# Kernel optimization log

Measured on AMD Instinct MI355X. Metric: run time of the kernel, lower is better.

Reference implementation:

```python
import jax, jax.numpy as jnp
import numpy as np

# Production GravNet config: 8 events x 4096 hits, K=40 neighbours, 4 spatial dims
B, V, K, S, P, F_IN, F_OUT = 8, 4096, 40, 4, 64, 64, 128
N = B * V
MAX_RADIUS_SQ = 1.0  # SelectKnn(max_radius=1.0)


def setup_inputs() -> dict:
    key = jax.random.key(0)
    ks = jax.random.split(key, 7)
    x = jax.random.normal(ks[0], (N, F_IN), jnp.float32)
    # Dense layer params (glorot-ish scaling)
    W_prop = jax.random.normal(ks[1], (F_IN, P), jnp.float32) / np.sqrt(F_IN)
    b_prop = jnp.zeros((P,), jnp.float32)
    W_sp = jax.random.normal(ks[2], (F_IN, S), jnp.float32) / np.sqrt(F_IN)
    b_sp = jnp.zeros((S,), jnp.float32)
    # output transform input dim = n_prop_total (2*P) + F_IN
    W_out = jax.random.normal(ks[3], (2 * P + F_IN, F_OUT), jnp.float32) / np.sqrt(2 * P + F_IN)
    b_out = jnp.zeros((F_OUT,), jnp.float32)
    row_splits = jnp.arange(B + 1, dtype=jnp.int32) * V  # equal-size ragged segments
    return dict(x=x, W_prop=W_prop, b_prop=b_prop, W_sp=W_sp, b_sp=b_sp,
                W_out=W_out, b_out=b_out, row_splits=row_splits)


def _knn_indices(coords):
    """Per-event brute-force KNN. coords: [N,S] -> global neighbour idx [N,K]."""
    c = coords.reshape(B, V, S)
    # pairwise squared distances within each event: [B,V,V]
    d = jnp.sum((c[:, :, None, :] - c[:, None, :, :]) ** 2, axis=-1)
    neg_d, idx = jax.lax.top_k(-d, K + 1)  # nearest first; col 0 is self (d=0)
    idx, dsq = idx[:, :, 1:], -neg_d[:, :, 1:]
    # tf_compatible max_radius: out-of-radius neighbours -> self index
    self_idx = jnp.arange(V, dtype=idx.dtype)[None, :, None]
    idx = jnp.where(dsq > MAX_RADIUS_SQ, self_idx, idx)
    gidx = idx + (jnp.arange(B, dtype=idx.dtype) * V)[:, None, None]
    return gidx.reshape(N, K)


def reference(x, W_prop, b_prop, W_sp, b_sp, W_out, b_out, row_splits):
    coords = x @ W_sp + b_sp                      # [N,S] learned coordinates
    nidx = _knn_indices(coords)                   # [N,K] (int, non-diff)
    nb_coords = coords[nidx]                      # [N,K,S] gather
    dsq = jnp.sum((coords[:, None, :] - nb_coords) ** 2, axis=-1)  # [N,K]
    feat = x @ W_prop + b_prop                    # [N,P]
    w = jnp.exp(-10.0 * dsq)[:, :, None]          # gauss_of_lin(10*d^2)
    nf = feat[nidx] * w                           # [N,K,P]
    agg = jnp.concatenate([nf.max(axis=1), nf.mean(axis=1)], axis=-1)  # [N,2P]
    out = jnp.tanh(jnp.concatenate([agg, x], axis=-1) @ W_out + b_out)  # [N,F_OUT]
    return out
```

## Files before the change

### kernel.cpp

```cpp
#include <hip/hip_runtime.h>
#include <cstdint>
#include <cstddef>

#define NB   8
#define VV   4096
#define KNN  40
#define NTOT 32768
#define CAP  224
#define INFB 0x7F800000u
#define ONEB 0x3F800000u

__device__ __forceinline__ int xbucket(float x) {
  int b = (int)floorf((x + 4.f) * 32.f);
  return b < 0 ? 0 : (b > 255 ? 255 : b);
}

__global__ __launch_bounds__(256) void k_prep(
    const float* __restrict__ x, const float* __restrict__ W_prop,
    const float* __restrict__ b_prop, const float* __restrict__ W_sp,
    const float* __restrict__ b_sp, const float* __restrict__ W_out,
    float* __restrict__ coords, float* __restrict__ feat,
    float* __restrict__ xW, int* __restrict__ hist)
{
  __shared__ float xt[64][64];
  const int t = threadIdx.x;
  const int row0 = blockIdx.x * 64;

  #pragma unroll
  for (int i = 0; i < 16; ++i) {
    int idx = t + i * 256;
    xt[idx >> 6][idx & 63] = x[(size_t)row0 * 64 + idx];
  }
  __syncthreads();

  {
    const int col = t & 63, rb = (t >> 6) * 16;
    float acc[16];
    #pragma unroll
    for (int i = 0; i < 16; ++i) acc[i] = b_prop[col];
    for (int k = 0; k < 64; k += 4) {
      const float w0 = W_prop[(k + 0) * 64 + col];
      const float w1 = W_prop[(k + 1) * 64 + col];
      const float w2 = W_prop[(k + 2) * 64 + col];
      const float w3 = W_prop[(k + 3) * 64 + col];
      #pragma unroll
      for (int i = 0; i < 16; ++i) {
        const float4 a4 = *(const float4*)&xt[rb + i][k];
        acc[i] += a4.x * w0 + a4.y * w1 + a4.z * w2 + a4.w * w3;
      }
    }
    #pragma unroll
    for (int i = 0; i < 16; ++i)
      feat[(size_t)(row0 + rb + i) * 64 + col] = acc[i];
  }

  {
    const int col = t & 127, who = t >> 7;
    #pragma unroll
    for (int p = 0; p < 2; ++p) {
      const int rb = who * 16 + p * 32;
      float acc[16];
      #pragma unroll
      for (int i = 0; i < 16; ++i) acc[i] = 0.f;
      for (int k = 0; k < 64; k += 4) {
        const float w0 = W_out[(size_t)(128 + k + 0) * 128 + col];
        const float w1 = W_out[(size_t)(128 + k + 1) * 128 + col];
        const float w2 = W_out[(size_t)(128 + k + 2) * 128 + col];
        const float w3 = W_out[(size_t)(128 + k + 3) * 128 + col];
        #pragma unroll
        for (int i = 0; i < 16; ++i) {
          const float4 a4 = *(const float4*)&xt[rb + i][k];
          acc[i] += a4.x * w0 + a4.y * w1 + a4.z * w2 + a4.w * w3;
        }
      }
      #pragma unroll
      for (int i = 0; i < 16; ++i)
        xW[(size_t)(row0 + rb + i) * 128 + col] = acc[i];
    }
  }

  if (t < 64) {
    float a0 = b_sp[0], a1 = b_sp[1], a2 = b_sp[2], a3 = b_sp[3];
    for (int k = 0; k < 64; ++k) {
      const float xv = xt[t][k];
      a0 += xv * W_sp[k * 4 + 0];
      a1 += xv * W_sp[k * 4 + 1];
      a2 += xv * W_sp[k * 4 + 2];
      a3 += xv * W_sp[k * 4 + 3];
    }
    ((float4*)coords)[row0 + t] = make_float4(a0, a1, a2, a3);
    const int ev = (row0 + t) >> 12;
    atomicAdd(&hist[ev * 256 + xbucket(a0)], 1);
  }
}

__global__ __launch_bounds__(512) void k_scatter(
    const float* __restrict__ coords, float* __restrict__ csort,
    unsigned short* __restrict__ perm, const int* __restrict__ hist,
    int* __restrict__ cursorDelta, unsigned short* __restrict__ prefg)
{
  __shared__ int pref[257];
  const int t = threadIdx.x;
  const int ev = blockIdx.x >> 3;
  const int i = ((blockIdx.x & 7) << 9) + t;
  const int evbase = ev * VV;

  if (t < 64) {
    const int* h = hist + ev * 256;
    const int l = t;
    const int h0 = h[4*l], h1 = h[4*l+1], h2 = h[4*l+2], h3 = h[4*l+3];
    const int s = h0 + h1 + h2 + h3;
    int incl = s;
    #pragma unroll
    for (int off = 1; off < 64; off <<= 1) {
      const int v = __shfl_up(incl, off);
      if (l >= off) incl += v;
    }
    const int excl = incl - s;
    pref[4*l]   = excl;
    pref[4*l+1] = excl + h0;
    pref[4*l+2] = excl + h0 + h1;
    pref[4*l+3] = excl + h0 + h1 + h2;
    if (l == 63) pref[256] = excl + s;
  }
  __syncthreads();

  const float4 c = ((const float4*)coords)[evbase + i];
  const int b = xbucket(c.x);
  const int pos = pref[b] + atomicAdd(&cursorDelta[ev * 256 + b], 1);
  ((float4*)csort)[evbase + pos] = c;
  perm[evbase + pos] = (unsigned short)i;

  if ((blockIdx.x & 7) == 0 && t < 257)
    prefg[ev * 257 + t] = (unsigned short)pref[t];
}

template <int NC>
__device__ __forceinline__ unsigned bs40(const uint2* __restrict__ list,
                                         int M, int lane) {
  unsigned dv[NC];
  #pragma unroll
  for (int j = 0; j < NC; ++j) {
    const int e = lane + j * 64;
    dv[j] = (e < M) ? list[e].x : INFB;
  }
  unsigned lo = 0, hi = ONEB;
  while (lo < hi) {
    const unsigned mid = (lo + hi) >> 1;
    int cnt = 0;
    #pragma unroll
    for (int j = 0; j < NC; ++j)
      cnt += (int)__popcll(__ballot(dv[j] <= mid));
    if (cnt >= KNN) hi = mid; else lo = mid + 1;
  }
  return hi;
}

#define AGG_CHUNK(J0, N)                                                     \
  {                                                                          \
    float fv[N], wgt[N];                                                     \
    _Pragma("unroll")                                                        \
    for (int j = 0; j < N; ++j) {                                            \
      const uint2 en = list[(J0) + j];                                       \
      wgt[j] = __expf(-10.f * __uint_as_float(en.x));                        \
      const int ei = __builtin_amdgcn_readfirstlane((int)en.y);              \
      fv[j] = fe[(size_t)ei * 64 + lane];                                    \
    }                                                                        \
    _Pragma("unroll")                                                        \
    for (int j = 0; j < N; ++j) {                                            \
      const float v = fv[j] * wgt[j];                                        \
      vmax = fmaxf(vmax, v);                                                 \
      vsum += v;                                                             \
    }                                                                        \
  }

__global__ __launch_bounds__(512, 4) void k_knn(
    const float* __restrict__ coords,
    const unsigned short* __restrict__ perm,
    const unsigned short* __restrict__ prefg,
    const float* __restrict__ feat, float* __restrict__ agg)
{
  __shared__ float4 cs[VV];
  __shared__ uint2 lists[8][CAP];
  __shared__ unsigned short pr[257];

  const int t = threadIdx.x, lane = t & 63;
  const int wvid = __builtin_amdgcn_readfirstlane(t) >> 6;
  const int bid0 = blockIdx.x;
  const int bid = (bid0 & 7) * 64 + (bid0 >> 3);
  const int ev = bid >> 6;
  const int slot = bid & 63;
  const int evbase = ev * VV;

  {
    const float4* cg = (const float4*)coords + evbase;
    for (int i = t; i < VV; i += 512) cs[i] = cg[i];
    if (t < 257) pr[t] = prefg[ev * 257 + t];
  }
  __syncthreads();

  uint2* list = lists[wvid];
  const float* fe = feat + (size_t)evbase * 64;
  const unsigned long long lmask = (1ull << lane) - 1ull;

  auto scan = [&](unsigned rbits, int q, float4 qc, int lo, int hi) -> int {
    int M = 0;
    #pragma unroll 4
    for (int base = lo; base < hi; base += 64) {
      const int c = base + lane;
      const float4 cc = cs[c];
      const float dx = qc.x - cc.x, dy = qc.y - cc.y;
      const float dz = qc.z - cc.z, dw = qc.w - cc.w;
      const float dsq = dx * dx + dy * dy + dz * dz + dw * dw;
      const bool pred = (__float_as_uint(dsq) <= rbits) && (c != q);
      const unsigned long long bm = __ballot(pred);
      if (pred) {
        const int pos = M + (int)__popcll(bm & lmask);
        if (pos < CAP)
          list[pos] = make_uint2(__float_as_uint(dsq), (unsigned)c);
      }
      M += (int)__popcll(bm);
    }
    return M;
  };

  for (int qi = 0; qi < 8; ++qi) {
    const int q = slot + (qi * 8 + wvid) * 64;
    const float4 qc = cs[q];
    const int origq = (int)perm[evbase + q];
    const int bq = xbucket(qc.x);
    const int wlo = ((int)pr[bq > 32 ? bq - 32 : 0]) & ~63;
    const int whi0 = (int)pr[bq + 33 > 256 ? 256 : bq + 33];
    const int whi = (whi0 + 63) & ~63;

    int M = scan(ONEB, q, qc, wlo, whi);
    bool ok = true;

    if (M > CAP) {
      const unsigned t0 = bs40<4>(list, CAP, lane);
      M = scan(t0, q, qc, wlo, whi);
      ok = (M <= CAP);
    }

    float vmax = -__builtin_inff(), vsum = 0.f;

    if (ok) {
      for (int be = 0; be < M; be += 64) {
        const int e = be + lane;
        if (e < M) {
          uint2 en = list[e];
          en.y = (unsigned)perm[evbase + (int)en.y];
          list[e] = en;
        }
      }

      int Msel;
      if (M > KNN) {
        unsigned taub;
        if      (M <=  64) taub = bs40<1>(list, M, lane);
        else if (M <= 128) taub = bs40<2>(list, M, lane);
        else               taub = bs40<4>(list, M, lane);
        int S = 0;
        for (int be = 0; be < M; be += 64) {
          const int e = be + lane;
          uint2 en = make_uint2(0u, 0u);
          bool p = false;
          if (e < M) { en = list[e]; p = (en.x <= taub); }
          const unsigned long long bm = __ballot(p);
          if (p) list[S + (int)__popcll(bm & lmask)] = en;
          S += (int)__popcll(bm);
        }
        Msel = S;
      } else {
        if (lane >= M && lane < KNN)
          list[lane] = make_uint2(0u, (unsigned)origq);
        Msel = KNN;
      }

      if (Msel == KNN) {
        AGG_CHUNK(0, 16)
        AGG_CHUNK(16, 16)
        AGG_CHUNK(32, 8)
      } else {
        #pragma unroll 4
        for (int e = 0; e < Msel; ++e) {
          const uint2 en = list[e];
          const int ei = __builtin_amdgcn_readfirstlane((int)en.y);
          const float w = __expf(-10.f * __uint_as_float(en.x));
          const float v = fe[(size_t)ei * 64 + lane] * w;
          vmax = fmaxf(vmax, v);
          vsum += v;
        }
      }
    } else {
      unsigned lo = 0, hi = ONEB;
      while (lo < hi) {
        const unsigned mid = (lo + hi) >> 1;
        const float fm = __uint_as_float(mid);
        int cnt = 0;
        for (int base = wlo; base < whi; base += 64) {
          const int c = base + lane;
          const float4 cc = cs[c];
          const float dx = qc.x - cc.x, dy = qc.y - cc.y;
          const float dz = qc.z - cc.z, dw = qc.w - cc.w;
          const float dsq = dx * dx + dy * dy + dz * dz + dw * dw;
          cnt += (int)__popcll(__ballot(dsq <= fm && c != q));
        }
        if (cnt >= KNN) hi = mid; else lo = mid + 1;
      }
      const float tau = __uint_as_float(hi);
      for (int c = wlo; c < whi; ++c) {
        if (c == q) continue;
        const float4 cc = cs[c];
        const float dx = qc.x - cc.x, dy = qc.y - cc.y;
        const float dz = qc.z - cc.z, dw = qc.w - cc.w;
        const float dsq = dx * dx + dy * dy + dz * dz + dw * dw;
        if (dsq <= tau) {
          const int ei = (int)perm[evbase + c];
          const float w = __expf(-10.f * dsq);
          const float v = fe[(size_t)ei * 64 + lane] * w;
          vmax = fmaxf(vmax, v);
          vsum += v;
        }
      }
    }

    const int g = evbase + origq;
    agg[(size_t)g * 128 + lane]      = vmax;
    agg[(size_t)g * 128 + 64 + lane] = vsum * (1.f / 40.f);
  }
}

__global__ __launch_bounds__(256) void k_out(
    const float* __restrict__ agg, const float* __restrict__ W_out,
    const float* __restrict__ b_out, float* __restrict__ out)
{
  __shared__ float at[64][128];
  const int t = threadIdx.x;
  const int row0 = blockIdx.x * 64;

  #pragma unroll
  for (int i = 0; i < 32; ++i) {
    int idx = t + i * 256;
    at[idx >> 7][idx & 127] = agg[(size_t)row0 * 128 + idx];
  }
  __syncthreads();

  const int col = t & 127, who = t >> 7;
  #pragma unroll
  for (int p = 0; p < 2; ++p) {
    const int rb = who * 16 + p * 32;
    float acc[16];
    #pragma unroll
    for (int i = 0; i < 16; ++i) acc[i] = 0.f;
    for (int k = 0; k < 128; k += 4) {
      const float w0 = W_out[(size_t)(k + 0) * 128 + col];
      const float w1 = W_out[(size_t)(k + 1) * 128 + col];
      const float w2 = W_out[(size_t)(k + 2) * 128 + col];
      const float w3 = W_out[(size_t)(k + 3) * 128 + col];
      #pragma unroll
      for (int i = 0; i < 16; ++i) {
        const float4 a4 = *(const float4*)&at[rb + i][k];
        acc[i] += a4.x * w0 + a4.y * w1 + a4.z * w2 + a4.w * w3;
      }
    }
    const float bb = b_out[col];
    #pragma unroll
    for (int i = 0; i < 16; ++i) {
      const size_t o = (size_t)(row0 + rb + i) * 128 + col;
      float v = acc[i] + bb + out[o];
      v = fminf(15.f, fmaxf(-15.f, v));
      const float e = __expf(2.f * v);
      out[o] = (e - 1.f) / (e + 1.f);
    }
  }
}

extern "C" void kernel_launch(void* const* d_in, const int* in_sizes, int n_in,
                              void* d_out, int out_size, void* d_ws, size_t ws_size,
                              hipStream_t stream) {
  const float* x      = (const float*)d_in[0];
  const float* W_prop = (const float*)d_in[1];
  const float* b_prop = (const float*)d_in[2];
  const float* W_sp   = (const float*)d_in[3];
  const float* b_sp   = (const float*)d_in[4];
  const float* W_out  = (const float*)d_in[5];
  const float* b_out  = (const float*)d_in[6];

  float* out = (float*)d_out;
  char* ws = (char*)d_ws;
  float* coords          = (float*)(ws);
  float* csort           = (float*)(ws + (512 << 10));
  float* feat            = (float*)(ws + (1 << 20));
  float* agg             = (float*)(ws + (9 << 20));
  unsigned short* perm   = (unsigned short*)(ws + (25 << 20));
  unsigned short* prefg  = (unsigned short*)(ws + (25 << 20) + 65536);
  int* hist              = (int*)(ws + (25 << 20) + 65536 + 4608);
  int* cursorDelta       = (int*)(ws + (25 << 20) + 65536 + 4608 + 8192);

  hipMemsetAsync(hist, 0, 16384, stream);
  k_prep<<<NTOT / 64, 256, 0, stream>>>(x, W_prop, b_prop, W_sp, b_sp, W_out,
                                        coords, feat, out ,
                                        hist);
  k_scatter<<<NB * 8, 512, 0, stream>>>(coords, csort, perm, hist,
                                        cursorDelta, prefg);
  k_knn<<<NB * (VV / 64), 512, 0, stream>>>(csort, perm, prefg, feat, agg);
  k_out<<<NTOT / 64, 256, 0, stream>>>(agg, W_out, b_out, out);
}
```

Before: 184.9 us.

## Replace 1D x-bucket sort with 2D x-slab/y-bin grid for KNN candidate pruning

Changes the spatial binning from 256 fine x-buckets to a 16x32 grid of coarse x-slabs by y-bins. Each query now scans only the y-bin range within radius 1 inside each nearby x-slab, rather than a contiguous x-window. This cuts the number of candidate distance evaluations per query in the radius scan, the overflow rescan and the fallback path. The cost is a per-slab loop with small ranges that may waste more of each 64-lane chunk, and a larger histogram and prefix table.

```diff
diff --git a/kernel.cpp b/kernel.cpp
--- a/kernel.cpp
+++ b/kernel.cpp
@@ -10,9 +10,13 @@
 #define INFB 0x7F800000u
 #define ONEB 0x3F800000u
 
-__device__ __forceinline__ int xbucket(float x) {
-  int b = (int)floorf((x + 4.f) * 32.f);
-  return b < 0 ? 0 : (b > 255 ? 255 : b);
+__device__ __forceinline__ int slabf(float x) {
+  int b = (int)floorf((x + 4.f) * 2.f);
+  return b < 0 ? 0 : (b > 15 ? 15 : b);
+}
+__device__ __forceinline__ int ybf(float y) {
+  int b = (int)floorf((y + 4.f) * 4.f);
+  return b < 0 ? 0 : (b > 31 ? 31 : b);
 }
 
 __global__ __launch_bounds__(256) void k_prep(
@@ -90,7 +94,7 @@
     }
     ((float4*)coords)[row0 + t] = make_float4(a0, a1, a2, a3);
     const int ev = (row0 + t) >> 12;
-    atomicAdd(&hist[ev * 256 + xbucket(a0)], 1);
+    atomicAdd(&hist[ev * 512 + slabf(a0) * 32 + ybf(a1)], 1);
   }
 }
 
@@ -99,40 +103,41 @@
     unsigned short* __restrict__ perm, const int* __restrict__ hist,
     int* __restrict__ cursorDelta, unsigned short* __restrict__ prefg)
 {
-  __shared__ int pref[257];
+  __shared__ int pref[513];
   const int t = threadIdx.x;
   const int ev = blockIdx.x >> 3;
   const int i = ((blockIdx.x & 7) << 9) + t;
   const int evbase = ev * VV;
 
   if (t < 64) {
-    const int* h = hist + ev * 256;
     const int l = t;
-    const int h0 = h[4*l], h1 = h[4*l+1], h2 = h[4*l+2], h3 = h[4*l+3];
-    const int s = h0 + h1 + h2 + h3;
+    const int* h = hist + ev * 512 + 8 * l;
+    int hv[8], s = 0;
+    #pragma unroll
+    for (int j = 0; j < 8; ++j) { hv[j] = h[j]; s += hv[j]; }
     int incl = s;
     #pragma unroll
     for (int off = 1; off < 64; off <<= 1) {
       const int v = __shfl_up(incl, off);
       if (l >= off) incl += v;
     }
-    const int excl = incl - s;
-    pref[4*l]   = excl;
-    pref[4*l+1] = excl + h0;
-    pref[4*l+2] = excl + h0 + h1;
-    pref[4*l+3] = excl + h0 + h1 + h2;
-    if (l == 63) pref[256] = excl + s;
+    int run = incl - s;
+    #pragma unroll
+    for (int j = 0; j < 8; ++j) { pref[8 * l + j] = run; run += hv[j]; }
+    if (l == 63) pref[512] = run;
   }
   __syncthreads();
 
   const float4 c = ((const float4*)coords)[evbase + i];
-  const int b = xbucket(c.x);
-  const int pos = pref[b] + atomicAdd(&cursorDelta[ev * 256 + b], 1);
+  const int key = slabf(c.x) * 32 + ybf(c.y);
+  const int pos = pref[key] + atomicAdd(&cursorDelta[ev * 512 + key], 1);
   ((float4*)csort)[evbase + pos] = c;
   perm[evbase + pos] = (unsigned short)i;
 
-  if ((blockIdx.x & 7) == 0 && t < 257)
-    prefg[ev * 257 + t] = (unsigned short)pref[t];
+  if ((blockIdx.x & 7) == 0) {
+    prefg[ev * 513 + t] = (unsigned short)pref[t];
+    if (t == 0) prefg[ev * 513 + 512] = (unsigned short)pref[512];
+  }
 }
 
 template <int NC>
@@ -182,7 +187,7 @@
 {
   __shared__ float4 cs[VV];
   __shared__ uint2 lists[8][CAP];
-  __shared__ unsigned short pr[257];
+  __shared__ unsigned short pr[513];
 
   const int t = threadIdx.x, lane = t & 63;
   const int wvid = __builtin_amdgcn_readfirstlane(t) >> 6;
@@ -195,7 +200,7 @@
   {
     const float4* cg = (const float4*)coords + evbase;
     for (int i = t; i < VV; i += 512) cs[i] = cg[i];
-    if (t < 257) pr[t] = prefg[ev * 257 + t];
+    for (int i = t; i < 513; i += 512) pr[i] = prefg[ev * 513 + i];
   }
   __syncthreads();
 
@@ -203,23 +208,31 @@
   const float* fe = feat + (size_t)evbase * 64;
   const unsigned long long lmask = (1ull << lane) - 1ull;
 
-  auto scan = [&](unsigned rbits, int q, float4 qc, int lo, int hi) -> int {
-    int M = 0;
-    #pragma unroll 4
-    for (int base = lo; base < hi; base += 64) {
-      const int c = base + lane;
-      const float4 cc = cs[c];
-      const float dx = qc.x - cc.x, dy = qc.y - cc.y;
-      const float dz = qc.z - cc.z, dw = qc.w - cc.w;
-      const float dsq = dx * dx + dy * dy + dz * dz + dw * dw;
-      const bool pred = (__float_as_uint(dsq) <= rbits) && (c != q);
-      const unsigned long long bm = __ballot(pred);
-      if (pred) {
-        const int pos = M + (int)__popcll(bm & lmask);
-        if (pos < CAP)
-          list[pos] = make_uint2(__float_as_uint(dsq), (unsigned)c);
-      }
-      M += (int)__popcll(bm);
+  auto scanAll = [&](unsigned rbits, int q, float4 qc,
+                     int slo, int shi, int yblo, int ybhi) -> int {
+    int M = 0, pend = 0;
+    for (int s = slo; s <= shi; ++s) {
+      int alo = ((int)pr[(s << 5) + yblo]) & ~63;
+      int ahi = (((int)pr[(s << 5) + ybhi + 1]) + 63) & ~63;
+      alo = alo < pend ? pend : alo;
+      if (ahi < alo) ahi = alo;
+      pend = ahi;
+      #pragma unroll 4
+      for (int base = alo; base < ahi; base += 64) {
+        const int c = base + lane;
+        const float4 cc = cs[c];
+        const float dx = qc.x - cc.x, dy = qc.y - cc.y;
+        const float dz = qc.z - cc.z, dw = qc.w - cc.w;
+        const float dsq = dx * dx + dy * dy + dz * dz + dw * dw;
+        const bool pred = (__float_as_uint(dsq) <= rbits) && (c != q);
+        const unsigned long long bm = __ballot(pred);
+        if (pred) {
+          const int pos = M + (int)__popcll(bm & lmask);
+          if (pos < CAP)
+            list[pos] = make_uint2(__float_as_uint(dsq), (unsigned)c);
+        }
+        M += (int)__popcll(bm);
+      }
     }
     return M;
   };
@@ -228,17 +241,15 @@
     const int q = slot + (qi * 8 + wvid) * 64;
     const float4 qc = cs[q];
     const int origq = (int)perm[evbase + q];
-    const int bq = xbucket(qc.x);
-    const int wlo = ((int)pr[bq > 32 ? bq - 32 : 0]) & ~63;
-    const int whi0 = (int)pr[bq + 33 > 256 ? 256 : bq + 33];
-    const int whi = (whi0 + 63) & ~63;
-
-    int M = scan(ONEB, q, qc, wlo, whi);
+    const int slo = slabf(qc.x - 1.f), shi = slabf(qc.x + 1.f);
+    const int yblo = ybf(qc.y - 1.f),  ybhi = ybf(qc.y + 1.f);
+
+    int M = scanAll(ONEB, q, qc, slo, shi, yblo, ybhi);
     bool ok = true;
 
     if (M > CAP) {
       const unsigned t0 = bs40<4>(list, CAP, lane);
-      M = scan(t0, q, qc, wlo, whi);
+      M = scanAll(t0, q, qc, slo, shi, yblo, ybhi);
       ok = (M <= CAP);
     }
 
@@ -297,30 +308,45 @@
       while (lo < hi) {
         const unsigned mid = (lo + hi) >> 1;
         const float fm = __uint_as_float(mid);
-        int cnt = 0;
-        for (int base = wlo; base < whi; base += 64) {
-          const int c = base + lane;
+        int cnt = 0, pend = 0;
+        for (int s = slo; s <= shi; ++s) {
+          int alo = ((int)pr[(s << 5) + yblo]) & ~63;
+          int ahi = (((int)pr[(s << 5) + ybhi + 1]) + 63) & ~63;
+          alo = alo < pend ? pend : alo;
+          if (ahi < alo) ahi = alo;
+          pend = ahi;
+          for (int base = alo; base < ahi; base += 64) {
+            const int c = base + lane;
+            const float4 cc = cs[c];
+            const float dx = qc.x - cc.x, dy = qc.y - cc.y;
+            const float dz = qc.z - cc.z, dw = qc.w - cc.w;
+            const float dsq = dx * dx + dy * dy + dz * dz + dw * dw;
+            cnt += (int)__popcll(__ballot(dsq <= fm && c != q));
+          }
+        }
+        if (cnt >= KNN) hi = mid; else lo = mid + 1;
+      }
+      const float tau = __uint_as_float(hi);
+      int pend = 0;
+      for (int s = slo; s <= shi; ++s) {
+        int alo = ((int)pr[(s << 5) + yblo]) & ~63;
+        int ahi = (((int)pr[(s << 5) + ybhi + 1]) + 63) & ~63;
+        alo = alo < pend ? pend : alo;
+        if (ahi < alo) ahi = alo;
+        pend = ahi;
+        for (int c = alo; c < ahi; ++c) {
+          if (c == q) continue;
           const float4 cc = cs[c];
           const float dx = qc.x - cc.x, dy = qc.y - cc.y;
           const float dz = qc.z - cc.z, dw = qc.w - cc.w;
           const float dsq = dx * dx + dy * dy + dz * dz + dw * dw;
-          cnt += (int)__popcll(__ballot(dsq <= fm && c != q));
-        }
-        if (cnt >= KNN) hi = mid; else lo = mid + 1;
-      }
-      const float tau = __uint_as_float(hi);
-      for (int c = wlo; c < whi; ++c) {
-        if (c == q) continue;
-        const float4 cc = cs[c];
-        const float dx = qc.x - cc.x, dy = qc.y - cc.y;
-        const float dz = qc.z - cc.z, dw = qc.w - cc.w;
-        const float dsq = dx * dx + dy * dy + dz * dz + dw * dw;
-        if (dsq <= tau) {
-          const int ei = (int)perm[evbase + c];
-          const float w = __expf(-10.f * dsq);
-          const float v = fe[(size_t)ei * 64 + lane] * w;
-          vmax = fmaxf(vmax, v);
-          vsum += v;
+          if (dsq <= tau) {
+            const int ei = (int)perm[evbase + c];
+            const float w = __expf(-10.f * dsq);
+            const float v = fe[(size_t)ei * 64 + lane] * w;
+            vmax = fmaxf(vmax, v);
+            vsum += v;
+          }
         }
       }
     }
@@ -395,10 +421,10 @@
   float* agg             = (float*)(ws + (9 << 20));
   unsigned short* perm   = (unsigned short*)(ws + (25 << 20));
   unsigned short* prefg  = (unsigned short*)(ws + (25 << 20) + 65536);
-  int* hist              = (int*)(ws + (25 << 20) + 65536 + 4608);
-  int* cursorDelta       = (int*)(ws + (25 << 20) + 65536 + 4608 + 8192);
-
-  hipMemsetAsync(hist, 0, 16384, stream);
+  int* hist              = (int*)(ws + (25 << 20) + 65536 + 8704);
+  int* cursorDelta       = (int*)(ws + (25 << 20) + 65536 + 8704 + 16384);
+
+  hipMemsetAsync(hist, 0, 32768, stream);
   k_prep<<<NTOT / 64, 256, 0, stream>>>(x, W_prop, b_prop, W_sp, b_sp, W_out,
                                         coords, feat, out ,
                                         hist);
```

New measurement: 184.2 us. About the same (-0.4%).
